# Optimization experiments

Hardware: AMD Instinct MI355X
Metric: run time of the kernel (lower is better)

## Reference

```python
import jax, jax.numpy as jnp
import numpy as np

B, H, S, D = 4, 16, 2048, 64


def setup_inputs() -> dict:
    key = jax.random.key(0)
    kq, kk, kv = jax.random.split(key, 3)
    Q = jax.random.normal(kq, (B, H, S, D), dtype=jnp.float32)
    K = jax.random.normal(kk, (B, H, S, D), dtype=jnp.float32)
    V = jax.random.normal(kv, (B, H, S, D), dtype=jnp.float32)
    mask = jnp.ones((1, 1, S, S), dtype=jnp.int32)
    return {"Q": Q, "K": K, "V": V, "mask": mask}


def reference(Q, K, V, mask):
    d_k = Q.shape[-1]
    scale = 1.0 / jnp.sqrt(jnp.asarray(d_k, dtype=Q.dtype))
    # [B, H, S, S] attention scores
    attn = jnp.einsum('bhqd,bhkd->bhqk', Q, K) * scale
    # mask == 0 -> -1e9 (matches torch boolean-index assignment)
    attn = jnp.where(mask == 0, jnp.asarray(-1e9, dtype=attn.dtype), attn)
    softmax_attn = jax.nn.softmax(attn, axis=-1)
    out = jnp.einsum('bhqk,bhkd->bhqd', softmax_attn, V)
    return out
```

## Files before the change

### kernel.cpp

```cpp
#include <hip/hip_runtime.h>

typedef __bf16 bf16;
typedef __attribute__((ext_vector_type(8))) __bf16 bf16x8;
typedef __attribute__((ext_vector_type(8))) ushort ushort8v;
typedef __attribute__((ext_vector_type(4))) ushort ushort4v;
typedef __attribute__((ext_vector_type(16))) float f32x16;

constexpr int S_LEN = 2048;
constexpr int DH    = 64;
constexpr int QBLK  = 128;
constexpr int KVBLK = 64;
constexpr int NWAVE = 4;
constexpr int NT    = S_LEN / KVBLK;
constexpr float QSCALE = 0.125f * 1.44269504088896f;
constexpr float NEG    = -1.44269504e9f;
constexpr float THR    = 8.0f;
constexpr size_t TILE_BYTES = (size_t)KVBLK * DH * 2;
constexpr size_t KV_BYTES   = (size_t)64 * NT * TILE_BYTES;

__device__ __forceinline__ ushort bfb(float f) {
  bf16 b = (bf16)f;
  return __builtin_bit_cast(ushort, b);
}
__device__ __forceinline__ int SWZ(int row) {
  return ((row & 7) ^ ((row >> 3) & 7)) << 4;
}
__device__ __forceinline__ uint cvtpk(float lo, float hi) {
  uint r;
  asm("v_cvt_pk_bf16_f32 %0, %1, %2" : "=v"(r) : "v"(lo), "v"(hi));
  return r;
}
__device__ __forceinline__ void gload16(const char* g, void* l) {
  __builtin_amdgcn_global_load_lds(
      (__attribute__((address_space(1))) void*)(g),
      (__attribute__((address_space(3))) void*)(l), 16, 0, 0);
}

__global__ __launch_bounds__(256)
void mask_flags(const int* __restrict__ M, uint* __restrict__ F) {
  const int qt  = blockIdx.x;
  const int kt0 = blockIdx.y * 4;
  const int tid = threadIdx.x;
  const int r  = tid >> 2;
  const int c0 = (tid & 3) * 16;
  __shared__ int s[4];
  uint bits = 0;
  for (int i = 0; i < 4; ++i) {
    const int kt = kt0 + i;
    const int* row = M + (size_t)(qt * 64 + r) * S_LEN + kt * 64 + c0;
    int ok = 1;
#pragma unroll
    for (int j = 0; j < 4; ++j) {
      int4 v = *(const int4*)(row + j * 4);
      ok &= (v.x != 0) & (v.y != 0) & (v.z != 0) & (v.w != 0);
    }
    ok = __all(ok) ? 1 : 0;
    if ((tid & 63) == 0) s[tid >> 6] = ok;
    __syncthreads();
    if (s[0] & s[1] & s[2] & s[3]) bits |= 1u << kt;
    __syncthreads();
  }
  if (tid == 0) atomicOr(&F[qt], bits);
}

__global__ __launch_bounds__(256)
void cvt_kv(const float* __restrict__ K, const float* __restrict__ V,
            char* __restrict__ kws, char* __restrict__ vws) {
  const int t = blockIdx.x, bh = blockIdx.y, tid = threadIdx.x;
  const float* Kb = K + ((size_t)bh * S_LEN + t * KVBLK) * DH;
  const float* Vb = V + ((size_t)bh * S_LEN + t * KVBLK) * DH;
  char* kd = kws + ((size_t)bh * NT + t) * TILE_BYTES;
  char* vd = vws + ((size_t)bh * NT + t) * TILE_BYTES;

  const int kr0 = tid >> 3, kc8 = tid & 7;
#pragma unroll
  for (int h = 0; h < 2; ++h) {
    const int row = kr0 + 32 * h;
    const float* kp = Kb + (size_t)row * DH + kc8 * 8;
    float4 a = *(const float4*)kp;
    float4 b = *(const float4*)(kp + 4);
    ushort8v pk;
    pk[0]=bfb(a.x); pk[1]=bfb(a.y); pk[2]=bfb(a.z); pk[3]=bfb(a.w);
    pk[4]=bfb(b.x); pk[5]=bfb(b.y); pk[6]=bfb(b.z); pk[7]=bfb(b.w);
    *(ushort8v*)(kd + row * 128 + ((kc8 * 16) ^ SWZ(row))) = pk;
  }
  const int vr = (tid >> 4) * 4, vc = (tid & 15) * 4;
  float rr[4][4];
#pragma unroll
  for (int i = 0; i < 4; ++i)
    *(float4*)rr[i] = *(const float4*)(Vb + (size_t)(vr + i) * DH + vc);
#pragma unroll
  for (int c = 0; c < 4; ++c) {
    const int d = vc + c;
    ushort4v p4;
    p4[0]=bfb(rr[0][c]); p4[1]=bfb(rr[1][c]);
    p4[2]=bfb(rr[2][c]); p4[3]=bfb(rr[3][c]);
    *(ushort4v*)(vd + d * 128 + ((vr * 2) ^ SWZ(d))) = p4;
  }
}

template<bool PRE>
__global__ __launch_bounds__(256, 4)
void attn_fwd(const float* __restrict__ Q, const float* __restrict__ K,
              const float* __restrict__ V, const int* __restrict__ M,
              const uint* __restrict__ F, const char* __restrict__ kws,
              const char* __restrict__ vws, float* __restrict__ O)
{
  __shared__ __align__(16) ushort kb[KVBLK * DH];
  __shared__ __align__(16) ushort vb[DH * KVBLK];

  const int tid  = threadIdx.x;
  const int lane = tid & 63;
  const int w    = tid >> 6;
  const int ql   = lane & 31;
  const int h    = lane >> 5;

  const int flat = blockIdx.y * gridDim.x + blockIdx.x;
  const int nid  = (flat & 7) * 128 + (flat >> 3);
  const int q0   = (nid & 15) * QBLK;
  const int bh   = nid >> 4;

  const float* Qb = Q + ((size_t)bh * S_LEN) * DH;
  const float* Kb = K + ((size_t)bh * S_LEN) * DH;
  const float* Vb = V + ((size_t)bh * S_LEN) * DH;

  const uint fmask = PRE ? (F[(q0 >> 6)] & F[(q0 >> 6) + 1]) : 0u;

  bf16x8 qf[4];
  {
    const float* qp = Qb + (size_t)(q0 + w * 32 + ql) * DH + 8 * h;
#pragma unroll
    for (int s = 0; s < 4; ++s) {
      float4 a = *(const float4*)(qp + 16 * s);
      float4 b = *(const float4*)(qp + 16 * s + 4);
      bf16x8 t2;
      t2[0]=(bf16)(a.x*QSCALE); t2[1]=(bf16)(a.y*QSCALE);
      t2[2]=(bf16)(a.z*QSCALE); t2[3]=(bf16)(a.w*QSCALE);
      t2[4]=(bf16)(b.x*QSCALE); t2[5]=(bf16)(b.y*QSCALE);
      t2[6]=(bf16)(b.z*QSCALE); t2[7]=(bf16)(b.w*QSCALE);
      qf[s] = t2;
    }
  }

  f32x16 acc0, acc1;
#pragma unroll
  for (int i = 0; i < 16; ++i) { acc0[i] = 0.f; acc1[i] = 0.f; }
  float mrow = -1e30f;
  float rsum = 0.f;

  int kofs[2][4];
#pragma unroll
  for (int x = 0; x < 2; ++x) {
    const int row = 32 * x + ql;
    const int sw  = SWZ(row);
#pragma unroll
    for (int s = 0; s < 4; ++s)
      kofs[x][s] = row * 128 + ((32 * s + 16 * h) ^ sw);
  }

  auto mkfrag = [&](float p0, float p1, float p2, float p3,
                    float p4, float p5, float p6, float p7) -> bf16x8 {
    uint a0 = cvtpk(p0, p1), a1 = cvtpk(p2, p3);
    uint b0 = cvtpk(p4, p5), b1 = cvtpk(p6, p7);
    uint ta0 = __shfl_xor(a0, 32), ta1 = __shfl_xor(a1, 32);
    uint tb0 = __shfl_xor(b0, 32), tb1 = __shfl_xor(b1, 32);
    uint4 wv;
    wv.x = h ? tb0 : a0;
    wv.y = h ? tb1 : a1;
    wv.z = h ? b0  : ta0;
    wv.w = h ? b1  : ta1;
    return __builtin_bit_cast(bf16x8, wv);
  };

  const int kr0 = tid >> 3, kc8 = tid & 7;
  const int vr = (tid >> 4) * 4, vc = (tid & 15) * 4;

  for (int t = 0; t < NT; ++t) {
    if (PRE) {
      const char* ksrc = kws + ((size_t)bh * NT + t) * TILE_BYTES;
      const char* vsrc = vws + ((size_t)bh * NT + t) * TILE_BYTES;
#pragma unroll
      for (int c = 0; c < 2; ++c) {
        const int off = (w + c * 4) * 1024 + lane * 16;
        gload16(ksrc + off, (char*)kb + off);
        gload16(vsrc + off, (char*)vb + off);
      }
    } else {
#pragma unroll
      for (int hh = 0; hh < 2; ++hh) {
        const int row = kr0 + 32 * hh;
        const float* kp = Kb + (size_t)(t * KVBLK + row) * DH + kc8 * 8;
        float4 a = *(const float4*)kp;
        float4 b = *(const float4*)(kp + 4);
        ushort8v pk;
        pk[0]=bfb(a.x); pk[1]=bfb(a.y); pk[2]=bfb(a.z); pk[3]=bfb(a.w);
        pk[4]=bfb(b.x); pk[5]=bfb(b.y); pk[6]=bfb(b.z); pk[7]=bfb(b.w);
        *(ushort8v*)((char*)kb + row * 128 + ((kc8 * 16) ^ SWZ(row))) = pk;
      }
      float rr[4][4];
#pragma unroll
      for (int i = 0; i < 4; ++i)
        *(float4*)rr[i] = *(const float4*)(Vb + (size_t)(t * KVBLK + vr + i) * DH + vc);
#pragma unroll
      for (int c = 0; c < 4; ++c) {
        const int d = vc + c;
        ushort4v p4;
        p4[0]=bfb(rr[0][c]); p4[1]=bfb(rr[1][c]);
        p4[2]=bfb(rr[2][c]); p4[3]=bfb(rr[3][c]);
        *(ushort4v*)((char*)vb + d * 128 + ((vr * 2) ^ SWZ(d))) = p4;
      }
    }
    __syncthreads();

    f32x16 sc0, sc1;
#pragma unroll
    for (int i = 0; i < 16; ++i) { sc0[i] = 0.f; sc1[i] = 0.f; }

    __builtin_amdgcn_s_setprio(1);
#pragma unroll
    for (int s = 0; s < 4; ++s) {
      bf16x8 k0 = *(const bf16x8*)((const char*)kb + kofs[0][s]);
      bf16x8 k1 = *(const bf16x8*)((const char*)kb + kofs[1][s]);
      sc0 = __builtin_amdgcn_mfma_f32_32x32x16_bf16(k0, qf[s], sc0, 0,0,0);
      sc1 = __builtin_amdgcn_mfma_f32_32x32x16_bf16(k1, qf[s], sc1, 0,0,0);
    }
    __builtin_amdgcn_s_setprio(0);

    const bool allset = PRE ? (((fmask >> t) & 1u) != 0u) : false;
    if (!allset) {
      const size_t mo = (size_t)(q0 + w * 32 + ql) * S_LEN + t * KVBLK + 4 * h;
#pragma unroll
      for (int r = 0; r < 16; ++r) {
        const int cr = (r & 3) + 8 * (r >> 2);
        if (M[mo + cr] == 0)      sc0[r] = NEG;
        if (M[mo + 32 + cr] == 0) sc1[r] = NEG;
      }
    }

    float lm = fmaxf(sc0[0], sc0[1]);
#pragma unroll
    for (int i = 2; i < 16; ++i) lm = fmaxf(lm, sc0[i]);
#pragma unroll
    for (int i = 0; i < 16; ++i) lm = fmaxf(lm, sc1[i]);
    lm = fmaxf(lm, __shfl_xor(lm, 32));

    if (!__all(lm - mrow <= THR)) {
      const float mnew = fmaxf(mrow, lm);
      const float corr = __builtin_amdgcn_exp2f(mrow - mnew);
      rsum *= corr;
      acc0 *= corr;
      acc1 *= corr;
      mrow = mnew;
    }

    float ps = 0.f;
#pragma unroll
    for (int i = 0; i < 16; ++i) {
      sc0[i] = __builtin_amdgcn_exp2f(sc0[i] - mrow); ps += sc0[i];
      sc1[i] = __builtin_amdgcn_exp2f(sc1[i] - mrow); ps += sc1[i];
    }
    rsum += ps;

    bf16x8 pf[4];
    pf[0] = mkfrag(sc0[0], sc0[1], sc0[2],  sc0[3],  sc0[4],  sc0[5],  sc0[6],  sc0[7]);
    pf[1] = mkfrag(sc0[8], sc0[9], sc0[10], sc0[11], sc0[12], sc0[13], sc0[14], sc0[15]);
    pf[2] = mkfrag(sc1[0], sc1[1], sc1[2],  sc1[3],  sc1[4],  sc1[5],  sc1[6],  sc1[7]);
    pf[3] = mkfrag(sc1[8], sc1[9], sc1[10], sc1[11], sc1[12], sc1[13], sc1[14], sc1[15]);

    __builtin_amdgcn_s_setprio(1);
#pragma unroll
    for (int s = 0; s < 4; ++s) {
      bf16x8 v0 = *(const bf16x8*)((const char*)vb + kofs[0][s]);
      bf16x8 v1 = *(const bf16x8*)((const char*)vb + kofs[1][s]);
      acc0 = __builtin_amdgcn_mfma_f32_32x32x16_bf16(v0, pf[s], acc0, 0,0,0);
      acc1 = __builtin_amdgcn_mfma_f32_32x32x16_bf16(v1, pf[s], acc1, 0,0,0);
    }
    __builtin_amdgcn_s_setprio(0);

    __syncthreads();
  }

  rsum += __shfl_xor(rsum, 32);
  const float inv = 1.0f / rsum;
  float* Ob = O + ((size_t)bh * S_LEN + q0 + w * 32 + ql) * DH + 4 * h;
#pragma unroll
  for (int g = 0; g < 4; ++g) {
    float4 o0 = { acc0[4*g+0]*inv, acc0[4*g+1]*inv, acc0[4*g+2]*inv, acc0[4*g+3]*inv };
    float4 o1 = { acc1[4*g+0]*inv, acc1[4*g+1]*inv, acc1[4*g+2]*inv, acc1[4*g+3]*inv };
    *(float4*)(Ob + 8 * g)      = o0;
    *(float4*)(Ob + 32 + 8 * g) = o1;
  }
}

extern "C" void kernel_launch(void* const* d_in, const int* in_sizes, int n_in,
                              void* d_out, int out_size, void* d_ws, size_t ws_size,
                              hipStream_t stream)
{
  const float* Q = (const float*)d_in[0];
  const float* K = (const float*)d_in[1];
  const float* V = (const float*)d_in[2];
  const int*   M = (const int*)d_in[3];
  float* O = (float*)d_out;

  const size_t need = 4096 + 2 * KV_BYTES;
  const bool pre = (d_ws != nullptr) && (ws_size >= need);

  dim3 grid(S_LEN / QBLK, 4 * 16);
  if (pre) {
    uint* F   = (uint*)d_ws;
    char* kws = (char*)d_ws + 4096;
    char* vws = kws + KV_BYTES;
    hipMemsetAsync(F, 0, 32 * sizeof(uint), stream);
    mask_flags<<<dim3(32, 8), 256, 0, stream>>>(M, F);
    cvt_kv<<<dim3(NT, 64), 256, 0, stream>>>(K, V, kws, vws);
    attn_fwd<true><<<grid, NWAVE * 64, 0, stream>>>(Q, K, V, M, F, kws, vws, O);
  } else {
    attn_fwd<false><<<grid, NWAVE * 64, 0, stream>>>(Q, K, V, M, nullptr, nullptr, nullptr, O);
  }
}
```

Measured before the change: 123.8 us.

## Double-buffer K/V LDS tiles to overlap async global loads with compute

Splits the K/V shared-memory tiles into two buffers. In the precomputed-workspace path, the direct global-to-LDS load for tile t+1 is issued before computing tile t, which cuts one barrier per tile and hides load latency behind the MFMA and softmax work. It also rewrites the row-max reduction as a tree instead of a serial chain. LDS use doubles to 32KB per block, which may limit occupancy at 4 blocks per CU.

After: 168.4 us. 36.1% more time.

```diff
diff --git a/kernel.cpp b/kernel.cpp
--- a/kernel.cpp
+++ b/kernel.cpp
@@ -106,8 +106,8 @@
               const uint* __restrict__ F, const char* __restrict__ kws,
               const char* __restrict__ vws, float* __restrict__ O)
 {
-  __shared__ __align__(16) ushort kb[KVBLK * DH];
-  __shared__ __align__(16) ushort vb[DH * KVBLK];
+  __shared__ __align__(16) ushort kb[2][KVBLK * DH];
+  __shared__ __align__(16) ushort vb[2][KVBLK * DH];
 
   const int tid  = threadIdx.x;
   const int lane = tid & 63;
@@ -172,20 +172,101 @@
     return __builtin_bit_cast(bf16x8, wv);
   };
 
-  const int kr0 = tid >> 3, kc8 = tid & 7;
-  const int vr = (tid >> 4) * 4, vc = (tid & 15) * 4;
-
-  for (int t = 0; t < NT; ++t) {
-    if (PRE) {
+  auto compute = [&](int t, const ushort* kbB, const ushort* vbB) {
+    f32x16 sc0, sc1;
+#pragma unroll
+    for (int i = 0; i < 16; ++i) { sc0[i] = 0.f; sc1[i] = 0.f; }
+
+    __builtin_amdgcn_s_setprio(1);
+#pragma unroll
+    for (int s = 0; s < 4; ++s) {
+      bf16x8 k0 = *(const bf16x8*)((const char*)kbB + kofs[0][s]);
+      bf16x8 k1 = *(const bf16x8*)((const char*)kbB + kofs[1][s]);
+      sc0 = __builtin_amdgcn_mfma_f32_32x32x16_bf16(k0, qf[s], sc0, 0,0,0);
+      sc1 = __builtin_amdgcn_mfma_f32_32x32x16_bf16(k1, qf[s], sc1, 0,0,0);
+    }
+    __builtin_amdgcn_s_setprio(0);
+
+    const bool allset = PRE ? (((fmask >> t) & 1u) != 0u) : false;
+    if (!allset) {
+      const size_t mo = (size_t)(q0 + w * 32 + ql) * S_LEN + t * KVBLK + 4 * h;
+#pragma unroll
+      for (int r = 0; r < 16; ++r) {
+        const int cr = (r & 3) + 8 * (r >> 2);
+        if (M[mo + cr] == 0)      sc0[r] = NEG;
+        if (M[mo + 32 + cr] == 0) sc1[r] = NEG;
+      }
+    }
+
+    float m0[8];
+#pragma unroll
+    for (int i = 0; i < 8; ++i)
+      m0[i] = fmaxf(fmaxf(sc0[i], sc0[i + 8]), fmaxf(sc1[i], sc1[i + 8]));
+    float m1a = fmaxf(fmaxf(m0[0], m0[1]), fmaxf(m0[2], m0[3]));
+    float m1b = fmaxf(fmaxf(m0[4], m0[5]), fmaxf(m0[6], m0[7]));
+    float lm  = fmaxf(m1a, m1b);
+    lm = fmaxf(lm, __shfl_xor(lm, 32));
+
+    if (!__all(lm - mrow <= THR)) {
+      const float mnew = fmaxf(mrow, lm);
+      const float corr = __builtin_amdgcn_exp2f(mrow - mnew);
+      rsum *= corr;
+      acc0 *= corr;
+      acc1 *= corr;
+      mrow = mnew;
+    }
+
+    float ps = 0.f;
+#pragma unroll
+    for (int i = 0; i < 16; ++i) {
+      sc0[i] = __builtin_amdgcn_exp2f(sc0[i] - mrow); ps += sc0[i];
+      sc1[i] = __builtin_amdgcn_exp2f(sc1[i] - mrow); ps += sc1[i];
+    }
+    rsum += ps;
+
+    bf16x8 pf[4];
+    pf[0] = mkfrag(sc0[0], sc0[1], sc0[2],  sc0[3],  sc0[4],  sc0[5],  sc0[6],  sc0[7]);
+    pf[1] = mkfrag(sc0[8], sc0[9], sc0[10], sc0[11], sc0[12], sc0[13], sc0[14], sc0[15]);
+    pf[2] = mkfrag(sc1[0], sc1[1], sc1[2],  sc1[3],  sc1[4],  sc1[5],  sc1[6],  sc1[7]);
+    pf[3] = mkfrag(sc1[8], sc1[9], sc1[10], sc1[11], sc1[12], sc1[13], sc1[14], sc1[15]);
+
+    __builtin_amdgcn_s_setprio(1);
+#pragma unroll
+    for (int s = 0; s < 4; ++s) {
+      bf16x8 v0 = *(const bf16x8*)((const char*)vbB + kofs[0][s]);
+      bf16x8 v1 = *(const bf16x8*)((const char*)vbB + kofs[1][s]);
+      acc0 = __builtin_amdgcn_mfma_f32_32x32x16_bf16(v0, pf[s], acc0, 0,0,0);
+      acc1 = __builtin_amdgcn_mfma_f32_32x32x16_bf16(v1, pf[s], acc1, 0,0,0);
+    }
+    __builtin_amdgcn_s_setprio(0);
+  };
+
+  if constexpr (PRE) {
+    auto issue = [&](int b, int t) {
       const char* ksrc = kws + ((size_t)bh * NT + t) * TILE_BYTES;
       const char* vsrc = vws + ((size_t)bh * NT + t) * TILE_BYTES;
 #pragma unroll
       for (int c = 0; c < 2; ++c) {
         const int off = (w + c * 4) * 1024 + lane * 16;
-        gload16(ksrc + off, (char*)kb + off);
-        gload16(vsrc + off, (char*)vb + off);
+        gload16(ksrc + off, (char*)kb[b] + off);
+        gload16(vsrc + off, (char*)vb[b] + off);
       }
-    } else {
+    };
+
+    issue(0, 0);
+    __syncthreads();
+    for (int t = 0; t < NT; t += 2) {
+      issue(1, t + 1);
+      compute(t, kb[0], vb[0]);
+      __syncthreads();
+      if (t + 2 < NT) issue(0, t + 2);
+      compute(t + 1, kb[1], vb[1]);
+      __syncthreads();
+    }
+  } else {
+    const int kr0 = tid >> 3, kc8 = tid & 7;
+    const int vr = (tid >> 4) * 4, vc = (tid & 15) * 4;
+    for (int t = 0; t < NT; ++t) {
 #pragma unroll
       for (int hh = 0; hh < 2; ++hh) {
         const int row = kr0 + 32 * hh;
@@ -195,7 +276,7 @@
         ushort8v pk;
         pk[0]=bfb(a.x); pk[1]=bfb(a.y); pk[2]=bfb(a.z); pk[3]=bfb(a.w);
         pk[4]=bfb(b.x); pk[5]=bfb(b.y); pk[6]=bfb(b.z); pk[7]=bfb(b.w);
-        *(ushort8v*)((char*)kb + row * 128 + ((kc8 * 16) ^ SWZ(row))) = pk;
+        *(ushort8v*)((char*)kb[0] + row * 128 + ((kc8 * 16) ^ SWZ(row))) = pk;
       }
       float rr[4][4];
 #pragma unroll
@@ -207,77 +288,12 @@
         ushort4v p4;
         p4[0]=bfb(rr[0][c]); p4[1]=bfb(rr[1][c]);
         p4[2]=bfb(rr[2][c]); p4[3]=bfb(rr[3][c]);
-        *(ushort4v*)((char*)vb + d * 128 + ((vr * 2) ^ SWZ(d))) = p4;
+        *(ushort4v*)((char*)vb[0] + d * 128 + ((vr * 2) ^ SWZ(d))) = p4;
       }
-    }
-    __syncthreads();
-
-    f32x16 sc0, sc1;
-#pragma unroll
-    for (int i = 0; i < 16; ++i) { sc0[i] = 0.f; sc1[i] = 0.f; }
-
-    __builtin_amdgcn_s_setprio(1);
-#pragma unroll
-    for (int s = 0; s < 4; ++s) {
-      bf16x8 k0 = *(const bf16x8*)((const char*)kb + kofs[0][s]);
-      bf16x8 k1 = *(const bf16x8*)((const char*)kb + kofs[1][s]);
-      sc0 = __builtin_amdgcn_mfma_f32_32x32x16_bf16(k0, qf[s], sc0, 0,0,0);
-      sc1 = __builtin_amdgcn_mfma_f32_32x32x16_bf16(k1, qf[s], sc1, 0,0,0);
-    }
-    __builtin_amdgcn_s_setprio(0);
-
-    const bool allset = PRE ? (((fmask >> t) & 1u) != 0u) : false;
-    if (!allset) {
-      const size_t mo = (size_t)(q0 + w * 32 + ql) * S_LEN + t * KVBLK + 4 * h;
-#pragma unroll
-      for (int r = 0; r < 16; ++r) {
-        const int cr = (r & 3) + 8 * (r >> 2);
-        if (M[mo + cr] == 0)      sc0[r] = NEG;
-        if (M[mo + 32 + cr] == 0) sc1[r] = NEG;
-      }
-    }
-
-    float lm = fmaxf(sc0[0], sc0[1]);
-#pragma unroll
-    for (int i = 2; i < 16; ++i) lm = fmaxf(lm, sc0[i]);
-#pragma unroll
-    for (int i = 0; i < 16; ++i) lm = fmaxf(lm, sc1[i]);
-    lm = fmaxf(lm, __shfl_xor(lm, 32));
-
-    if (!__all(lm - mrow <= THR)) {
-      const float mnew = fmaxf(mrow, lm);
-      const float corr = __builtin_amdgcn_exp2f(mrow - mnew);
-      rsum *= corr;
-      acc0 *= corr;
-      acc1 *= corr;
-      mrow = mnew;
-    }
-
-    float ps = 0.f;
-#pragma unroll
-    for (int i = 0; i < 16; ++i) {
-      sc0[i] = __builtin_amdgcn_exp2f(sc0[i] - mrow); ps += sc0[i];
-      sc1[i] = __builtin_amdgcn_exp2f(sc1[i] - mrow); ps += sc1[i];
-    }
-    rsum += ps;
-
-    bf16x8 pf[4];
-    pf[0] = mkfrag(sc0[0], sc0[1], sc0[2],  sc0[3],  sc0[4],  sc0[5],  sc0[6],  sc0[7]);
-    pf[1] = mkfrag(sc0[8], sc0[9], sc0[10], sc0[11], sc0[12], sc0[13], sc0[14], sc0[15]);
-    pf[2] = mkfrag(sc1[0], sc1[1], sc1[2],  sc1[3],  sc1[4],  sc1[5],  sc1[6],  sc1[7]);
-    pf[3] = mkfrag(sc1[8], sc1[9], sc1[10], sc1[11], sc1[12], sc1[13], sc1[14], sc1[15]);
-
-    __builtin_amdgcn_s_setprio(1);
-#pragma unroll
-    for (int s = 0; s < 4; ++s) {
-      bf16x8 v0 = *(const bf16x8*)((const char*)vb + kofs[0][s]);
-      bf16x8 v1 = *(const bf16x8*)((const char*)vb + kofs[1][s]);
-      acc0 = __builtin_amdgcn_mfma_f32_32x32x16_bf16(v0, pf[s], acc0, 0,0,0);
-      acc1 = __builtin_amdgcn_mfma_f32_32x32x16_bf16(v1, pf[s], acc1, 0,0,0);
-    }
-    __builtin_amdgcn_s_setprio(0);
-
-    __syncthreads();
+      __syncthreads();
+      compute(t, kb[0], vb[0]);
+      __syncthreads();
+    }
   }
 
   rsum += __shfl_xor(rsum, 32);
```
